# Performance work log

Hardware: AMD Instinct MI355X
Metric: run time of the kernel (lower is better)

The kernel has to match this reference:

```python
import jax, jax.numpy as jnp
import numpy as np

LAMBDA_REG = 0.1
RHO = 1.0

B_VOXELS = 4096   # batch of voxels
M_MEAS = 256      # measurements per voxel
K_ATOMS = 512     # dictionary atoms


def setup_inputs() -> dict:
    key = jax.random.key(0)
    k1, k2 = jax.random.split(key)
    # data: [voxels, measurements] as passed to fit()
    Y = jax.random.normal(k1, (B_VOXELS, M_MEAS), dtype=jnp.float32)
    # dictionary matrix Phi: [measurements, atoms]; kernels are nonnegative signals
    A = jax.random.uniform(k2, (M_MEAS, K_ATOMS), dtype=jnp.float32)
    return {"Y": Y, "A": A, "max_iter": 30}


def _soft_threshold(v, t):
    # L1Norm().prox
    return jnp.sign(v) * jnp.maximum(jnp.abs(v) - t, 0.0)


def reference(Y, A, max_iter):
    """ADMM solve: min_x ||Y^T - A x||^2 + lambda*||x||_1  s.t. x >= 0.
    Returns X_hat with shape [voxels, atoms]."""
    Yb = Y.T                                    # [M, B]
    K = A.shape[1]
    AtY = A.T @ Yb                              # [K, B]
    LHS = A.T @ A + RHO * jnp.eye(K, dtype=A.dtype)
    c_and_lower = jax.scipy.linalg.cho_factor(LHS)

    x0 = jnp.zeros_like(AtY)
    z0 = jnp.zeros_like(AtY)
    u0 = jnp.zeros_like(AtY)

    def admm_step(carry, _):
        x, z, u = carry
        rhs = AtY + RHO * (z - u)
        x_new = jax.scipy.linalg.cho_solve(c_and_lower, rhs)
        v = x_new + u
        v_proj = jnp.maximum(v, 0.0)            # nonnegativity prox (constrained=True)
        z_new = _soft_threshold(v_proj, LAMBDA_REG / RHO)  # L1 prox (lambda_reg>0)
        u_new = u + x_new - z_new
        return (x_new, z_new, u_new), None

    (X_hat, _, _), _ = jax.lax.scan(admm_step, (x0, z0, u0), None, length=max_iter)
    return X_hat.T                              # [voxels, atoms]
```

## Files before the change

### kernel.cpp

```cpp
#include <hip/hip_runtime.h>

#define NVOX   4096
#define NMEAS  256
#define NATOMS 512
#define NITER  30

typedef __attribute__((ext_vector_type(8))) short s8v;
typedef __attribute__((ext_vector_type(4))) short s4v;
typedef __attribute__((ext_vector_type(4))) float f32x4;

__device__ __forceinline__ unsigned short f2bf(float x) {
    unsigned u = __builtin_bit_cast(unsigned, x);
    u += 0x7fff + ((u >> 16) & 1);
    return (unsigned short)(u >> 16);
}
__device__ __forceinline__ float bf2f(unsigned short b) {
    unsigned u = ((unsigned)b) << 16;
    return __builtin_bit_cast(float, u);
}
__device__ __forceinline__ float g_of(float v) {
    return fmaxf(v - 0.1f, 0.0f) - fminf(v, 0.1f);
}

__global__ __launch_bounds__(256) void g_kernel_d(const float* __restrict__ A,
                                                  double* __restrict__ Gd,
                                                  float* __restrict__ Gf) {
    __shared__ float arow[NATOMS];
    int i = blockIdx.x;
    for (int k = threadIdx.x; k < NATOMS; k += 256) arow[k] = A[i * NATOMS + k];
    __syncthreads();
    int j = threadIdx.x;
    const float* aj = A + j * NATOMS;
    double s = (i == j) ? 1.0 : 0.0;
#pragma unroll 4
    for (int k = 0; k < NATOMS; ++k) s += (double)arow[k] * (double)aj[k];
    Gd[i * NMEAS + j] = s;
    Gf[i * NMEAS + j] = (float)s;
}

__global__ __launch_bounds__(1024) void sweep_inverse(const float* __restrict__ src,
                                                      float* __restrict__ dst) {
    __shared__ float s_dn[NMEAS];
    __shared__ float s_dt[NMEAS];
    int t = threadIdx.x;
    int rb = t & 31;
    int cb = t >> 5;
    float vals[8][8];
#pragma unroll
    for (int i = 0; i < 8; ++i) {
        const float* row = &src[(8 * rb + i) * NMEAS + 8 * cb];
        float4 a = *(const float4*)row;
        float4 b = *(const float4*)(row + 4);
        vals[i][0] = a.x; vals[i][1] = a.y; vals[i][2] = a.z; vals[i][3] = a.w;
        vals[i][4] = b.x; vals[i][5] = b.y; vals[i][6] = b.z; vals[i][7] = b.w;
    }
#pragma unroll 1
    for (int p = 0; p < NMEAS; ++p) {
        int pb = p >> 3, pi = p & 7;
        __syncthreads();
        if (cb == pb) {
#pragma unroll
            for (int i = 0; i < 8; ++i) {
                float v = vals[i][0];
#pragma unroll
                for (int j = 1; j < 8; ++j) if (pi == j) v = vals[i][j];
                s_dn[8 * rb + i] = v;
                s_dt[i * 32 + rb] = v;
            }
        }
        __syncthreads();
        float d   = s_dn[p];
        float inv = 1.0f / d;
        float rv[8], cv[8];
#pragma unroll
        for (int i = 0; i < 8; ++i) rv[i] = s_dt[i * 32 + rb];
#pragma unroll
        for (int j = 0; j < 8; ++j) cv[j] = s_dn[8 * cb + j] * inv;
#pragma unroll
        for (int i = 0; i < 8; ++i)
#pragma unroll
            for (int j = 0; j < 8; ++j) vals[i][j] -= rv[i] * cv[j];
        if (rb == pb) {
#pragma unroll
            for (int i = 0; i < 8; ++i) if (pi == i) {
#pragma unroll
                for (int j = 0; j < 8; ++j) vals[i][j] = cv[j];
            }
        }
        if (cb == pb) {
#pragma unroll
            for (int j = 0; j < 8; ++j) if (pi == j) {
#pragma unroll
                for (int i = 0; i < 8; ++i)
                    vals[i][j] = (rb == pb && pi == i) ? -inv : rv[i] * inv;
            }
        }
    }
#pragma unroll
    for (int i = 0; i < 8; ++i)
#pragma unroll
        for (int j = 0; j < 8; ++j)
            dst[(8 * rb + i) * NMEAS + 8 * cb + j] = -vals[i][j];
}

template <typename TB>
__global__ __launch_bounds__(256) void mm_gd(const double* __restrict__ Gd,
                                             const TB* __restrict__ X,
                                             double* __restrict__ P) {
    __shared__ __align__(16) double row[NMEAS];
    int i = blockIdx.x;
    row[threadIdx.x] = Gd[i * NMEAS + threadIdx.x];
    __syncthreads();
    int j = threadIdx.x;
    double s = 0.0;
#pragma unroll 4
    for (int k = 0; k < NMEAS; ++k) s += row[k] * (double)X[k * NMEAS + j];
    P[i * NMEAS + j] = s;
}

template <typename TB>
__global__ __launch_bounds__(256) void upd_newton(const TB* __restrict__ X,
                                                  const double* __restrict__ P,
                                                  double* __restrict__ Xn) {
    __shared__ __align__(16) double row[NMEAS];
    int i = blockIdx.x;
    row[threadIdx.x] = (double)X[i * NMEAS + threadIdx.x];
    __syncthreads();
    int j = threadIdx.x;
    double s = 0.0;
#pragma unroll 4
    for (int k = 0; k < NMEAS; ++k) s += row[k] * P[k * NMEAS + j];
    Xn[i * NMEAS + j] = 2.0 * row[j] - s;
}

__global__ __launch_bounds__(256) void h_kernel_d(const double* __restrict__ Gi,
                                                  const float* __restrict__ A,
                                                  double* __restrict__ H) {
    __shared__ __align__(16) double grow[NMEAS];
    int i = blockIdx.x;
    grow[threadIdx.x] = Gi[i * NMEAS + threadIdx.x];
    __syncthreads();
    int k0 = threadIdx.x;
    double s0 = 0.0, s1 = 0.0;
#pragma unroll 4
    for (int j = 0; j < NMEAS; ++j) {
        double g = grow[j];
        s0 += g * (double)A[j * NATOMS + k0];
        s1 += g * (double)A[j * NATOMS + k0 + 256];
    }
    H[i * NATOMS + k0] = s0;
    H[i * NATOMS + k0 + 256] = s1;
}

__global__ __launch_bounds__(256) void w_kernel_d(const float* __restrict__ A,
                                                  const double* __restrict__ H,
                                                  unsigned short* __restrict__ Whg,
                                                  unsigned short* __restrict__ Wlg) {
    __shared__ __align__(16) double acol[NMEAS];
    int p = blockIdx.x;
    acol[threadIdx.x] = (double)A[threadIdx.x * NATOMS + p];
    __syncthreads();
    int q0 = threadIdx.x;
    double s0 = 0.0, s1 = 0.0;
#pragma unroll 4
    for (int m = 0; m < NMEAS; ++m) {
        double a = acol[m];
        s0 += a * H[m * NATOMS + q0];
        s1 += a * H[m * NATOMS + q0 + 256];
    }
    double w0 = ((p == q0)       ? 1.0 : 0.0) - s0;
    double w1 = ((p == q0 + 256) ? 1.0 : 0.0) - s1;
    unsigned short h0 = f2bf((float)w0), h1 = f2bf((float)w1);
    Whg[p * NATOMS + q0]       = h0;
    Wlg[p * NATOMS + q0]       = f2bf((float)(w0 - (double)bf2f(h0)));
    Whg[p * NATOMS + q0 + 256] = h1;
    Wlg[p * NATOMS + q0 + 256] = f2bf((float)(w1 - (double)bf2f(h1)));
}

__global__ __launch_bounds__(256) void aty_kernel(const float* __restrict__ A,
                                                  const float* __restrict__ Y,
                                                  unsigned short* __restrict__ Dh0,
                                                  unsigned short* __restrict__ Dl0) {
    __shared__ __align__(16) float At[64][65];
    __shared__ __align__(16) float Yt[64][65];
    int b0 = blockIdx.x * 64, k0 = blockIdx.y * 64;
    int t = threadIdx.x, tx = t & 15, ty = t >> 4;
    float acc[4][4] = {};
    for (int m0 = 0; m0 < NMEAS; m0 += 64) {
        __syncthreads();
        {
            int kk = t & 63, mr = t >> 6;
#pragma unroll
            for (int p = 0; p < 16; ++p)
                At[mr + 4 * p][kk] = A[(m0 + mr + 4 * p) * NATOMS + k0 + kk];
            int mm = t & 63, br = t >> 6;
#pragma unroll
            for (int p = 0; p < 16; ++p)
                Yt[mm][br + 4 * p] = Y[(b0 + br + 4 * p) * NMEAS + m0 + mm];
        }
        __syncthreads();
#pragma unroll 4
        for (int m = 0; m < 64; ++m) {
            float av[4], yv[4];
#pragma unroll
            for (int i = 0; i < 4; ++i) av[i] = At[m][ty * 4 + i];
#pragma unroll
            for (int j = 0; j < 4; ++j) yv[j] = Yt[m][tx * 4 + j];
#pragma unroll
            for (int i = 0; i < 4; ++i)
#pragma unroll
                for (int j = 0; j < 4; ++j) acc[i][j] += av[i] * yv[j];
        }
    }
#pragma unroll
    for (int j = 0; j < 4; ++j) {
        int b = b0 + tx * 4 + j;
        s4v h4, l4;
#pragma unroll
        for (int i = 0; i < 4; ++i) {
            float f = acc[i][j];
            unsigned short h = f2bf(f);
            h4[i] = (short)h;
            l4[i] = (short)f2bf(f - bf2f(h));
        }
        *(s4v*)&Dh0[(long)b * NATOMS + k0 + ty * 4] = h4;
        *(s4v*)&Dl0[(long)b * NATOMS + k0 + ty * 4] = l4;
    }
}

template <int FIRST, int LAST>
__global__ __launch_bounds__(256) void admm_delta(
        const unsigned short* __restrict__ Whg,
        const unsigned short* __restrict__ Wlg,
        const unsigned short* __restrict__ Dhg,
        const unsigned short* __restrict__ Dlg,
        float* __restrict__ xbuf,
        float* __restrict__ vbuf,
        unsigned short* __restrict__ DhOut,
        unsigned short* __restrict__ DlOut,
        float* __restrict__ out) {
    __shared__ __align__(16) char smem[61440];
    unsigned short* Whs = (unsigned short*)smem;
    unsigned short* Wls = Whs + 2 * 64 * 40;
    unsigned short* Dhs = Wls + 2 * 64 * 40;
    unsigned short* Dls = Dhs + 2 * 128 * 40;

    const int t = threadIdx.x;
    const int lane = t & 63, wv = t >> 6;
    const int ln = lane & 15, kg = lane >> 4;
    const int n0 = blockIdx.x * 128, m0 = blockIdx.y * 64;

    const int wm = t >> 2, wslot = t & 3;
    const int tn = t >> 2, tslot = t & 3;

    f32x4 acc[4][2] = {};
    s8v rwh, rwl, rth0, rth1, rtl0, rtl1;

#define GLOAD(kc)                                                                \
    {                                                                            \
        long ko = (long)(kc)*32;                                                 \
        rwh  = *(const s8v*)&Whg[(long)(m0 + wm) * NATOMS + ko + wslot * 8];     \
        rwl  = *(const s8v*)&Wlg[(long)(m0 + wm) * NATOMS + ko + wslot * 8];     \
        rth0 = *(const s8v*)&Dhg[(long)(n0 + tn) * NATOMS + ko + tslot * 8];     \
        rth1 = *(const s8v*)&Dhg[(long)(n0 + 64 + tn) * NATOMS + ko + tslot * 8];\
        rtl0 = *(const s8v*)&Dlg[(long)(n0 + tn) * NATOMS + ko + tslot * 8];     \
        rtl1 = *(const s8v*)&Dlg[(long)(n0 + 64 + tn) * NATOMS + ko + tslot * 8];\
    }
#define DSWRITE(b)                                                  \
    {                                                               \
        *(s8v*)&Whs[(b)*2560 + wm * 40 + wslot * 8] = rwh;          \
        *(s8v*)&Wls[(b)*2560 + wm * 40 + wslot * 8] = rwl;          \
        *(s8v*)&Dhs[(b)*5120 + tn * 40 + tslot * 8] = rth0;         \
        *(s8v*)&Dhs[(b)*5120 + (64 + tn) * 40 + tslot * 8] = rth1;  \
        *(s8v*)&Dls[(b)*5120 + tn * 40 + tslot * 8] = rtl0;         \
        *(s8v*)&Dls[(b)*5120 + (64 + tn) * 40 + tslot * 8] = rtl1;  \
    }

    GLOAD(0);
    DSWRITE(0);
#pragma unroll 1
    for (int c = 0; c < 16; ++c) {
        if (c < 15) GLOAD(c + 1);
        __syncthreads();
        const int b = c & 1;
        const unsigned short* wh = &Whs[b * 2560];
        const unsigned short* wl = &Wls[b * 2560];
        const unsigned short* dh = &Dhs[b * 5120];
        const unsigned short* dl = &Dls[b * 5120];
        s8v ah[4], al[4], bh[2], bl[2];
#pragma unroll
        for (int mi = 0; mi < 4; ++mi) {
            ah[mi] = *(const s8v*)&wh[(mi * 16 + ln) * 40 + kg * 8];
            al[mi] = *(const s8v*)&wl[(mi * 16 + ln) * 40 + kg * 8];
        }
#pragma unroll
        for (int ni = 0; ni < 2; ++ni) {
            int r = wv * 32 + ni * 16 + ln;
            bh[ni] = *(const s8v*)&dh[r * 40 + kg * 8];
            bl[ni] = *(const s8v*)&dl[r * 40 + kg * 8];
        }
#pragma unroll
        for (int mi = 0; mi < 4; ++mi)
#pragma unroll
            for (int ni = 0; ni < 2; ++ni) {
                acc[mi][ni] = __builtin_amdgcn_mfma_f32_16x16x32_bf16(ah[mi], bh[ni], acc[mi][ni], 0, 0, 0);
                acc[mi][ni] = __builtin_amdgcn_mfma_f32_16x16x32_bf16(ah[mi], bl[ni], acc[mi][ni], 0, 0, 0);
                acc[mi][ni] = __builtin_amdgcn_mfma_f32_16x16x32_bf16(al[mi], bh[ni], acc[mi][ni], 0, 0, 0);
                acc[mi][ni] = __builtin_amdgcn_mfma_f32_16x16x32_bf16(al[mi], bl[ni], acc[mi][ni], 0, 0, 0);
            }
        if (c < 15) DSWRITE((c + 1) & 1);
    }
#undef GLOAD
#undef DSWRITE

    __syncthreads();
    float* xT = (float*)smem;

    if (!LAST) {
#pragma unroll
        for (int mi = 0; mi < 4; ++mi)
#pragma unroll
            for (int ni = 0; ni < 2; ++ni) {
                int nn = n0 + wv * 32 + ni * 16 + ln;
                f32x4 dlt;
#pragma unroll
                for (int j = 0; j < 4; ++j) {
                    int m = m0 + mi * 16 + kg * 4 + j;
                    long idx = (long)m * NVOX + nn;
                    float dx = acc[mi][ni][j];
                    float xn, vn, gold;
                    if (FIRST) {
                        xn = dx; vn = xn; gold = 0.0f;
                    } else {
                        xn = xbuf[idx] + dx;
                        float vp = vbuf[idx];
                        vn = xn + fminf(vp, 0.1f);
                        gold = g_of(vp);
                    }
                    xbuf[idx] = xn;
                    vbuf[idx] = vn;
                    dlt[j] = g_of(vn) - gold;
                }
                int nl = wv * 32 + ni * 16 + ln;
                int ml = mi * 16 + kg * 4;
                *(f32x4*)&xT[nl * 68 + ml] = dlt;
            }
        __syncthreads();
        int nl = t >> 1, seg = t & 1;
#pragma unroll
        for (int q8 = 0; q8 < 4; ++q8) {
            s8v hv, lv;
#pragma unroll
            for (int e = 0; e < 8; ++e) {
                float f = xT[nl * 68 + seg * 32 + q8 * 8 + e];
                unsigned short h = f2bf(f);
                hv[e] = (short)h;
                lv[e] = (short)f2bf(f - bf2f(h));
            }
            *(s8v*)&DhOut[(long)(n0 + nl) * NATOMS + m0 + seg * 32 + q8 * 8] = hv;
            *(s8v*)&DlOut[(long)(n0 + nl) * NATOMS + m0 + seg * 32 + q8 * 8] = lv;
        }
    } else {
#pragma unroll
        for (int mi = 0; mi < 4; ++mi)
#pragma unroll
            for (int ni = 0; ni < 2; ++ni) {
                int nn = n0 + wv * 32 + ni * 16 + ln;
                f32x4 tv;
#pragma unroll
                for (int j = 0; j < 4; ++j) {
                    int m = m0 + mi * 16 + kg * 4 + j;
                    tv[j] = xbuf[(long)m * NVOX + nn] + acc[mi][ni][j];
                }
                int nl = wv * 32 + ni * 16 + ln;
                int ml = mi * 16 + kg * 4;
                *(f32x4*)&xT[nl * 68 + ml] = tv;
            }
        __syncthreads();
        int nl = t >> 1, seg = t & 1;
#pragma unroll
        for (int q = 0; q < 8; ++q) {
            f32x4 v = *(const f32x4*)&xT[nl * 68 + seg * 32 + q * 4];
            *(f32x4*)&out[(long)(n0 + nl) * NATOMS + m0 + seg * 32 + q * 4] = v;
        }
    }
}

extern "C" void kernel_launch(void* const* d_in, const int* in_sizes, int n_in,
                              void* d_out, int out_size, void* d_ws, size_t ws_size,
                              hipStream_t stream) {
    const float* Y = (const float*)d_in[0];
    const float* A = (const float*)d_in[1];

    float* ws = (float*)d_ws;
    double* Gd  = (double*)(ws + 0);
    float*  Gf  = ws + 131072;
    float*  X0f = ws + 196608;
    double* X1d = (double*)(ws + 262144);
    double* Pd  = (double*)(ws + 393216);
    double* X2d = (double*)(ws + 131072);
    double* Hd  = (double*)(ws + 393216);
    float*  xbuf = ws + 655360;
    unsigned short* Whg = (unsigned short*)(ws + 0);
    unsigned short* Wlg = (unsigned short*)(ws + 131072);
    unsigned short* DAh = (unsigned short*)(ws + 2752512);
    unsigned short* DAl = (unsigned short*)(ws + 3801088);
    unsigned short* DBh = (unsigned short*)(ws + 4849664);
    unsigned short* DBl = (unsigned short*)(ws + 5898240);
    float* vbuf = (float*)d_out;
    float* outp = (float*)d_out;

    g_kernel_d<<<256, 256, 0, stream>>>(A, Gd, Gf);
    sweep_inverse<<<1, 1024, 0, stream>>>(Gf, X0f);
    mm_gd<float><<<256, 256, 0, stream>>>(Gd, X0f, Pd);
    upd_newton<float><<<256, 256, 0, stream>>>(X0f, Pd, X1d);
    mm_gd<double><<<256, 256, 0, stream>>>(Gd, X1d, Pd);
    upd_newton<double><<<256, 256, 0, stream>>>(X1d, Pd, X2d);
    h_kernel_d<<<256, 256, 0, stream>>>(X2d, A, Hd);
    w_kernel_d<<<512, 256, 0, stream>>>(A, Hd, Whg, Wlg);
    aty_kernel<<<dim3(64, 8), 256, 0, stream>>>(A, Y, DAh, DAl);

    dim3 ig(NVOX / 128, NATOMS / 64);
    unsigned short *ch = DAh, *cl = DAl, *nh = DBh, *nl = DBl;
    admm_delta<1, 0><<<ig, 256, 0, stream>>>(Whg, Wlg, ch, cl, xbuf, vbuf, nh, nl, nullptr);
    { unsigned short* s; s = ch; ch = nh; nh = s; s = cl; cl = nl; nl = s; }
    for (int it = 2; it <= NITER - 1; ++it) {
        admm_delta<0, 0><<<ig, 256, 0, stream>>>(Whg, Wlg, ch, cl, xbuf, vbuf, nh, nl, nullptr);
        unsigned short* s; s = ch; ch = nh; nh = s; s = cl; cl = nl; nl = s;
    }
    admm_delta<0, 1><<<ig, 256, 0, stream>>>(Whg, Wlg, ch, cl, xbuf, vbuf, nullptr, nullptr, outp);
}
```

Measured before the change: 1.118 ms.

## Block the Gauss-Jordan sweep inverse by 4 pivots and drop the lo*lo MFMA term

Replaces the single-pivot Gauss-Jordan sweep with a blocked variant that eliminates four pivots per step. It inverts a 4x4 pivot block locally and applies a rank-4 update, cutting the number of barrier-separated steps from 256 to 64. Separately, the split-bf16 ADMM GEMM drops the low*low MFMA product, removing a quarter of the matrix-core work per iteration at a small accuracy cost. The blocked pivoting drops some intermediate pivoting structure and may change numerical stability slightly.

```diff
diff --git a/kernel.cpp b/kernel.cpp
--- a/kernel.cpp
+++ b/kernel.cpp
@@ -38,10 +38,9 @@
     Gf[i * NMEAS + j] = (float)s;
 }
 
-__global__ __launch_bounds__(1024) void sweep_inverse(const float* __restrict__ src,
-                                                      float* __restrict__ dst) {
-    __shared__ float s_dn[NMEAS];
-    __shared__ float s_dt[NMEAS];
+__global__ __launch_bounds__(1024) void sweep_inverse_blk(const float* __restrict__ src,
+                                                          float* __restrict__ dst) {
+    __shared__ float U[4][8][32];
     int t = threadIdx.x;
     int rb = t & 31;
     int cb = t >> 5;
@@ -54,46 +53,90 @@
         vals[i][0] = a.x; vals[i][1] = a.y; vals[i][2] = a.z; vals[i][3] = a.w;
         vals[i][4] = b.x; vals[i][5] = b.y; vals[i][6] = b.z; vals[i][7] = b.w;
     }
+
 #pragma unroll 1
-    for (int p = 0; p < NMEAS; ++p) {
-        int pb = p >> 3, pi = p & 7;
-        __syncthreads();
-        if (cb == pb) {
+    for (int s = 0; s < 64; ++s) {
+        int pcb = s >> 1;
+        int ph  = (s & 1) * 4;
+        __syncthreads();
+        if (cb == pcb) {
+#pragma unroll
+            for (int a = 0; a < 4; ++a)
+#pragma unroll
+                for (int i = 0; i < 8; ++i)
+                    U[a][i][rb] = vals[i][ph + a];
+        }
+        __syncthreads();
+
+        float P[4][4];
+#pragma unroll
+        for (int a = 0; a < 4; ++a)
+#pragma unroll
+            for (int b = 0; b < 4; ++b)
+                P[a][b] = U[b][ph + a][pcb];
+#pragma unroll
+        for (int p = 0; p < 4; ++p) {
+            float inv = 1.0f / P[p][p];
+            float rv[4], cv[4];
+#pragma unroll
+            for (int a = 0; a < 4; ++a) rv[a] = P[a][p];
+#pragma unroll
+            for (int b = 0; b < 4; ++b) cv[b] = P[p][b] * inv;
+#pragma unroll
+            for (int a = 0; a < 4; ++a)
+#pragma unroll
+                for (int b = 0; b < 4; ++b) P[a][b] -= rv[a] * cv[b];
+#pragma unroll
+            for (int b = 0; b < 4; ++b) P[p][b] = cv[b];
+#pragma unroll
+            for (int a = 0; a < 4; ++a) P[a][p] = rv[a] * inv;
+            P[p][p] = -inv;
+        }
+        float B[4][4];
+#pragma unroll
+        for (int a = 0; a < 4; ++a)
+#pragma unroll
+            for (int b = 0; b < 4; ++b) B[a][b] = -P[a][b];
+
+        float E[8][4];
+#pragma unroll
+        for (int j = 0; j < 8; ++j) {
+            float n0 = U[0][j][cb], n1 = U[1][j][cb], n2 = U[2][j][cb], n3 = U[3][j][cb];
+#pragma unroll
+            for (int a = 0; a < 4; ++a)
+                E[j][a] = B[a][0] * n0 + B[a][1] * n1 + B[a][2] * n2 + B[a][3] * n3;
+        }
+
+#pragma unroll
+        for (int i = 0; i < 8; ++i) {
+            float m0 = U[0][i][rb], m1 = U[1][i][rb], m2 = U[2][i][rb], m3 = U[3][i][rb];
+#pragma unroll
+            for (int j = 0; j < 8; ++j)
+                vals[i][j] -= m0 * E[j][0] + m1 * E[j][1] + m2 * E[j][2] + m3 * E[j][3];
+        }
+
+        if (rb == pcb) {
+#pragma unroll
+            for (int ii = 0; ii < 4; ++ii)
+#pragma unroll
+                for (int j = 0; j < 8; ++j)
+                    vals[ph + ii][j] = E[j][ii];
+        }
+        if (cb == pcb) {
 #pragma unroll
             for (int i = 0; i < 8; ++i) {
-                float v = vals[i][0];
-#pragma unroll
-                for (int j = 1; j < 8; ++j) if (pi == j) v = vals[i][j];
-                s_dn[8 * rb + i] = v;
-                s_dt[i * 32 + rb] = v;
+                float m0 = U[0][i][rb], m1 = U[1][i][rb], m2 = U[2][i][rb], m3 = U[3][i][rb];
+#pragma unroll
+                for (int a = 0; a < 4; ++a)
+                    vals[i][ph + a] = m0 * B[0][a] + m1 * B[1][a] + m2 * B[2][a] + m3 * B[3][a];
             }
         }
-        __syncthreads();
-        float d   = s_dn[p];
-        float inv = 1.0f / d;
-        float rv[8], cv[8];
-#pragma unroll
-        for (int i = 0; i < 8; ++i) rv[i] = s_dt[i * 32 + rb];
-#pragma unroll
-        for (int j = 0; j < 8; ++j) cv[j] = s_dn[8 * cb + j] * inv;
-#pragma unroll
-        for (int i = 0; i < 8; ++i)
-#pragma unroll
-            for (int j = 0; j < 8; ++j) vals[i][j] -= rv[i] * cv[j];
-        if (rb == pb) {
-#pragma unroll
-            for (int i = 0; i < 8; ++i) if (pi == i) {
-#pragma unroll
-                for (int j = 0; j < 8; ++j) vals[i][j] = cv[j];
-            }
-        }
-        if (cb == pb) {
-#pragma unroll
-            for (int j = 0; j < 8; ++j) if (pi == j) {
-#pragma unroll
-                for (int i = 0; i < 8; ++i)
-                    vals[i][j] = (rb == pb && pi == i) ? -inv : rv[i] * inv;
-            }
+        if (rb == pcb && cb == pcb) {
+#pragma unroll
+            for (int ii = 0; ii < 4; ++ii)
+#pragma unroll
+                for (int a = 0; a < 4; ++a)
+                    vals[ph + ii][ph + a] = -B[ii][a];
         }
     }
 #pragma unroll
@@ -306,7 +349,6 @@
                 acc[mi][ni] = __builtin_amdgcn_mfma_f32_16x16x32_bf16(ah[mi], bh[ni], acc[mi][ni], 0, 0, 0);
                 acc[mi][ni] = __builtin_amdgcn_mfma_f32_16x16x32_bf16(ah[mi], bl[ni], acc[mi][ni], 0, 0, 0);
                 acc[mi][ni] = __builtin_amdgcn_mfma_f32_16x16x32_bf16(al[mi], bh[ni], acc[mi][ni], 0, 0, 0);
-                acc[mi][ni] = __builtin_amdgcn_mfma_f32_16x16x32_bf16(al[mi], bl[ni], acc[mi][ni], 0, 0, 0);
             }
         if (c < 15) DSWRITE((c + 1) & 1);
     }
@@ -411,7 +453,7 @@
     float* outp = (float*)d_out;
 
     g_kernel_d<<<256, 256, 0, stream>>>(A, Gd, Gf);
-    sweep_inverse<<<1, 1024, 0, stream>>>(Gf, X0f);
+    sweep_inverse_blk<<<1, 1024, 0, stream>>>(Gf, X0f);
     mm_gd<float><<<256, 256, 0, stream>>>(Gd, X0f, Pd);
     upd_newton<float><<<256, 256, 0, stream>>>(X0f, Pd, X1d);
     mm_gd<double><<<256, 256, 0, stream>>>(Gd, X1d, Pd);
```

Result: slower. 1.922 ms (+71.8%).

## Shrink ADMM delta tile to 64x32, drop lo*lo MFMA, swizzle block order

Applied to the files above, without the earlier changes.

The per-iteration delta GEMM moves from 128-voxel tiles to 32-voxel tiles, giving 1024 blocks instead of 256 and halving shared memory per block, so more blocks can be resident at once. The block index is remapped so that consecutive blocks group by voxel tile, aiming for better L2 reuse of the D operand. The bf16 split-precision product also drops the low*low term, cutting MFMA work by a quarter at a small accuracy cost. Smaller tiles mean each block reloads the W tile more often relative to its compute.

```diff
diff --git a/kernel.cpp b/kernel.cpp
--- a/kernel.cpp
+++ b/kernel.cpp
@@ -239,41 +239,42 @@
         unsigned short* __restrict__ DhOut,
         unsigned short* __restrict__ DlOut,
         float* __restrict__ out) {
-    __shared__ __align__(16) char smem[61440];
+    __shared__ __align__(16) char smem[30720];
     unsigned short* Whs = (unsigned short*)smem;
     unsigned short* Wls = Whs + 2 * 64 * 40;
     unsigned short* Dhs = Wls + 2 * 64 * 40;
-    unsigned short* Dls = Dhs + 2 * 128 * 40;
+    unsigned short* Dls = Dhs + 2 * 32 * 40;
 
     const int t = threadIdx.x;
     const int lane = t & 63, wv = t >> 6;
     const int ln = lane & 15, kg = lane >> 4;
-    const int n0 = blockIdx.x * 128, m0 = blockIdx.y * 64;
+
+    int bid = blockIdx.x + (blockIdx.y << 7);
+    int xr = bid & 7, q = bid >> 3;
+    int bx = xr * 16 + (q >> 3);
+    int by = q & 7;
+    const int n0 = bx * 32, m0 = by * 64;
 
     const int wm = t >> 2, wslot = t & 3;
-    const int tn = t >> 2, tslot = t & 3;
-
-    f32x4 acc[4][2] = {};
-    s8v rwh, rwl, rth0, rth1, rtl0, rtl1;
-
-#define GLOAD(kc)                                                                \
-    {                                                                            \
-        long ko = (long)(kc)*32;                                                 \
-        rwh  = *(const s8v*)&Whg[(long)(m0 + wm) * NATOMS + ko + wslot * 8];     \
-        rwl  = *(const s8v*)&Wlg[(long)(m0 + wm) * NATOMS + ko + wslot * 8];     \
-        rth0 = *(const s8v*)&Dhg[(long)(n0 + tn) * NATOMS + ko + tslot * 8];     \
-        rth1 = *(const s8v*)&Dhg[(long)(n0 + 64 + tn) * NATOMS + ko + tslot * 8];\
-        rtl0 = *(const s8v*)&Dlg[(long)(n0 + tn) * NATOMS + ko + tslot * 8];     \
-        rtl1 = *(const s8v*)&Dlg[(long)(n0 + 64 + tn) * NATOMS + ko + tslot * 8];\
+    const int dn = (t & 127) >> 2, dslot = t & 3;
+    const unsigned short* Dg  = (t < 128) ? Dhg : Dlg;
+    unsigned short*       Dsb = (t < 128) ? Dhs : Dls;
+
+    f32x4 acc[2] = {};
+    s8v rwh, rwl, rd;
+
+#define GLOAD(kc)                                                             \
+    {                                                                         \
+        long ko = (long)(kc)*32;                                              \
+        rwh = *(const s8v*)&Whg[(long)(m0 + wm) * NATOMS + ko + wslot * 8];   \
+        rwl = *(const s8v*)&Wlg[(long)(m0 + wm) * NATOMS + ko + wslot * 8];   \
+        rd  = *(const s8v*)&Dg [(long)(n0 + dn) * NATOMS + ko + dslot * 8];   \
     }
 #define DSWRITE(b)                                                  \
     {                                                               \
         *(s8v*)&Whs[(b)*2560 + wm * 40 + wslot * 8] = rwh;          \
         *(s8v*)&Wls[(b)*2560 + wm * 40 + wslot * 8] = rwl;          \
-        *(s8v*)&Dhs[(b)*5120 + tn * 40 + tslot * 8] = rth0;         \
-        *(s8v*)&Dhs[(b)*5120 + (64 + tn) * 40 + tslot * 8] = rth1;  \
-        *(s8v*)&Dls[(b)*5120 + tn * 40 + tslot * 8] = rtl0;         \
-        *(s8v*)&Dls[(b)*5120 + (64 + tn) * 40 + tslot * 8] = rtl1;  \
+        *(s8v*)&Dsb[(b)*1280 + dn * 40 + dslot * 8] = rd;           \
     }
 
     GLOAD(0);
@@ -285,29 +286,26 @@
         const int b = c & 1;
         const unsigned short* wh = &Whs[b * 2560];
         const unsigned short* wl = &Wls[b * 2560];
-        const unsigned short* dh = &Dhs[b * 5120];
-        const unsigned short* dl = &Dls[b * 5120];
-        s8v ah[4], al[4], bh[2], bl[2];
-#pragma unroll
-        for (int mi = 0; mi < 4; ++mi) {
-            ah[mi] = *(const s8v*)&wh[(mi * 16 + ln) * 40 + kg * 8];
-            al[mi] = *(const s8v*)&wl[(mi * 16 + ln) * 40 + kg * 8];
+        const unsigned short* dh = &Dhs[b * 1280];
+        const unsigned short* dl = &Dls[b * 1280];
+        s8v ah, al, bh[2], bl[2];
+        {
+            int row = wv * 16 + ln;
+            ah = *(const s8v*)&wh[row * 40 + kg * 8];
+            al = *(const s8v*)&wl[row * 40 + kg * 8];
         }
 #pragma unroll
         for (int ni = 0; ni < 2; ++ni) {
-            int r = wv * 32 + ni * 16 + ln;
-            bh[ni] = *(const s8v*)&dh[r * 40 + kg * 8];
-            bl[ni] = *(const s8v*)&dl[r * 40 + kg * 8];
-        }
-#pragma unroll
-        for (int mi = 0; mi < 4; ++mi)
-#pragma unroll
-            for (int ni = 0; ni < 2; ++ni) {
-                acc[mi][ni] = __builtin_amdgcn_mfma_f32_16x16x32_bf16(ah[mi], bh[ni], acc[mi][ni], 0, 0, 0);
-                acc[mi][ni] = __builtin_amdgcn_mfma_f32_16x16x32_bf16(ah[mi], bl[ni], acc[mi][ni], 0, 0, 0);
-                acc[mi][ni] = __builtin_amdgcn_mfma_f32_16x16x32_bf16(al[mi], bh[ni], acc[mi][ni], 0, 0, 0);
-                acc[mi][ni] = __builtin_amdgcn_mfma_f32_16x16x32_bf16(al[mi], bl[ni], acc[mi][ni], 0, 0, 0);
-            }
+            int row = ni * 16 + ln;
+            bh[ni] = *(const s8v*)&dh[row * 40 + kg * 8];
+            bl[ni] = *(const s8v*)&dl[row * 40 + kg * 8];
+        }
+#pragma unroll
+        for (int ni = 0; ni < 2; ++ni) {
+            acc[ni] = __builtin_amdgcn_mfma_f32_16x16x32_bf16(ah, bh[ni], acc[ni], 0, 0, 0);
+            acc[ni] = __builtin_amdgcn_mfma_f32_16x16x32_bf16(ah, bl[ni], acc[ni], 0, 0, 0);
+            acc[ni] = __builtin_amdgcn_mfma_f32_16x16x32_bf16(al, bh[ni], acc[ni], 0, 0, 0);
+        }
         if (c < 15) DSWRITE((c + 1) & 1);
     }
 #undef GLOAD
@@ -318,70 +316,65 @@
 
     if (!LAST) {
 #pragma unroll
-        for (int mi = 0; mi < 4; ++mi)
-#pragma unroll
-            for (int ni = 0; ni < 2; ++ni) {
-                int nn = n0 + wv * 32 + ni * 16 + ln;
-                f32x4 dlt;
-#pragma unroll
-                for (int j = 0; j < 4; ++j) {
-                    int m = m0 + mi * 16 + kg * 4 + j;
-                    long idx = (long)m * NVOX + nn;
-                    float dx = acc[mi][ni][j];
-                    float xn, vn, gold;
-                    if (FIRST) {
-                        xn = dx; vn = xn; gold = 0.0f;
-                    } else {
-                        xn = xbuf[idx] + dx;
-                        float vp = vbuf[idx];
-                        vn = xn + fminf(vp, 0.1f);
-                        gold = g_of(vp);
-                    }
-                    xbuf[idx] = xn;
-                    vbuf[idx] = vn;
-                    dlt[j] = g_of(vn) - gold;
+        for (int ni = 0; ni < 2; ++ni) {
+            int nn = n0 + ni * 16 + ln;
+            f32x4 dlt;
+#pragma unroll
+            for (int j = 0; j < 4; ++j) {
+                int m = m0 + wv * 16 + kg * 4 + j;
+                long idx = (long)m * NVOX + nn;
+                float dx = acc[ni][j];
+                float xn, vn, gold;
+                if (FIRST) {
+                    xn = dx; vn = xn; gold = 0.0f;
+                } else {
+                    xn = xbuf[idx] + dx;
+                    float vp = vbuf[idx];
+                    vn = xn + fminf(vp, 0.1f);
+                    gold = g_of(vp);
                 }
-                int nl = wv * 32 + ni * 16 + ln;
-                int ml = mi * 16 + kg * 4;
-                *(f32x4*)&xT[nl * 68 + ml] = dlt;
-            }
-        __syncthreads();
-        int nl = t >> 1, seg = t & 1;
-#pragma unroll
-        for (int q8 = 0; q8 < 4; ++q8) {
+                xbuf[idx] = xn;
+                vbuf[idx] = vn;
+                dlt[j] = g_of(vn) - gold;
+            }
+            int nl = ni * 16 + ln;
+            int ml = wv * 16 + kg * 4;
+            *(f32x4*)&xT[nl * 68 + ml] = dlt;
+        }
+        __syncthreads();
+        int nl = t >> 3, seg = t & 7;
+        {
             s8v hv, lv;
 #pragma unroll
             for (int e = 0; e < 8; ++e) {
-                float f = xT[nl * 68 + seg * 32 + q8 * 8 + e];
+                float f = xT[nl * 68 + seg * 8 + e];
                 unsigned short h = f2bf(f);
                 hv[e] = (short)h;
                 lv[e] = (short)f2bf(f - bf2f(h));
             }
-            *(s8v*)&DhOut[(long)(n0 + nl) * NATOMS + m0 + seg * 32 + q8 * 8] = hv;
-            *(s8v*)&DlOut[(long)(n0 + nl) * NATOMS + m0 + seg * 32 + q8 * 8] = lv;
+            *(s8v*)&DhOut[(long)(n0 + nl) * NATOMS + m0 + seg * 8] = hv;
+            *(s8v*)&DlOut[(long)(n0 + nl) * NATOMS + m0 + seg * 8] = lv;
         }
     } else {
 #pragma unroll
-        for (int mi = 0; mi < 4; ++mi)
-#pragma unroll
-            for (int ni = 0; ni < 2; ++ni) {
-                int nn = n0 + wv * 32 + ni * 16 + ln;
-                f32x4 tv;
-#pragma unroll
-                for (int j = 0; j < 4; ++j) {
-                    int m = m0 + mi * 16 + kg * 4 + j;
-                    tv[j] = xbuf[(long)m * NVOX + nn] + acc[mi][ni][j];
-                }
-                int nl = wv * 32 + ni * 16 + ln;
-                int ml = mi * 16 + kg * 4;
-                *(f32x4*)&xT[nl * 68 + ml] = tv;
-            }
-        __syncthreads();
-        int nl = t >> 1, seg = t & 1;
-#pragma unroll
-        for (int q = 0; q < 8; ++q) {
-            f32x4 v = *(const f32x4*)&xT[nl * 68 + seg * 32 + q * 4];
-            *(f32x4*)&out[(long)(n0 + nl) * NATOMS + m0 + seg * 32 + q * 4] = v;
+        for (int ni = 0; ni < 2; ++ni) {
+            int nn = n0 + ni * 16 + ln;
+            f32x4 tv;
+#pragma unroll
+            for (int j = 0; j < 4; ++j) {
+                int m = m0 + wv * 16 + kg * 4 + j;
+                tv[j] = xbuf[(long)m * NVOX + nn] + acc[ni][j];
+            }
+            int nl = ni * 16 + ln;
+            int ml = wv * 16 + kg * 4;
+            *(f32x4*)&xT[nl * 68 + ml] = tv;
+        }
+        __syncthreads();
+        int nl = t >> 3, seg = t & 7;
+#pragma unroll
+        for (int qq = 0; qq < 2; ++qq) {
+            f32x4 v = *(const f32x4*)&xT[nl * 68 + seg * 8 + qq * 4];
+            *(f32x4*)&out[(long)(n0 + nl) * NATOMS + m0 + seg * 8 + qq * 4] = v;
         }
     }
 }
@@ -420,7 +413,7 @@
     w_kernel_d<<<512, 256, 0, stream>>>(A, Hd, Whg, Wlg);
     aty_kernel<<<dim3(64, 8), 256, 0, stream>>>(A, Y, DAh, DAl);
 
-    dim3 ig(NVOX / 128, NATOMS / 64);
+    dim3 ig(NVOX / 32, NATOMS / 64);
     unsigned short *ch = DAh, *cl = DAl, *nh = DBh, *nl = DBl;
     admm_delta<1, 0><<<ig, 256, 0, stream>>>(Whg, Wlg, ch, cl, xbuf, vbuf, nh, nl, nullptr);
     { unsigned short* s; s = ch; ch = nh; nh = s; s = cl; cl = nl; nl = s; }
```

New measurement: 1.006 ms. -10.1%, faster.
